# Optimization experiments

Hardware: AMD Instinct MI355X
Metric: run time of the kernel (lower is better)

## Reference

```python
import jax, jax.numpy as jnp
import numpy as np

B, N, D_OBS, D_MSG, H = 4096, 64, 128, 64, 4
HD = D_MSG // H
EPS = 1e-5


def setup_inputs() -> dict:
    key = jax.random.key(0)
    ks = jax.random.split(key, 16)
    def w(k, shape):
        fan_in = shape[0]
        return (jax.random.normal(k, shape, dtype=jnp.float32) / np.sqrt(fan_in)).astype(jnp.float32)
    return {
        'obs_all': jax.random.normal(ks[0], (B, N, D_OBS), dtype=jnp.float32),
        # msg encoder: Linear(obs,128) -> ReLU -> Linear(128,msg)
        'enc_w1': w(ks[1], (D_OBS, 128)), 'enc_b1': jnp.zeros((128,), jnp.float32),
        'enc_w2': w(ks[2], (128, D_MSG)), 'enc_b2': jnp.zeros((D_MSG,), jnp.float32),
        # MultiheadAttention in/out projections (stored as (in, out))
        'in_proj_w': w(ks[3], (D_MSG, 3 * D_MSG)), 'in_proj_b': jnp.zeros((3 * D_MSG,), jnp.float32),
        'out_w': w(ks[4], (D_MSG, D_MSG)), 'out_b': jnp.zeros((D_MSG,), jnp.float32),
        # integrator: Linear(obs+msg,256) -> LayerNorm(256) -> ReLU -> Linear(256,obs)
        'int_w1': w(ks[5], (D_OBS + D_MSG, 256)), 'int_b1': jnp.zeros((256,), jnp.float32),
        'ln_g': jnp.ones((256,), jnp.float32), 'ln_b': jnp.zeros((256,), jnp.float32),
        'int_w2': w(ks[6], (256, D_OBS)), 'int_b2': jnp.zeros((D_OBS,), jnp.float32),
    }


def reference(obs_all, enc_w1, enc_b1, enc_w2, enc_b2,
              in_proj_w, in_proj_b, out_w, out_b,
              int_w1, int_b1, ln_g, ln_b, int_w2, int_b2):
    # --- send: encode observations into messages (B, N, msg_dim) ---
    h = jax.nn.relu(obs_all @ enc_w1 + enc_b1)
    msgs = h @ enc_w2 + enc_b2

    # --- attention aggregation: per-agent query over all messages.
    # The original per-agent loop (query = msgs[:, i:i+1]) is exactly
    # batched self-attention over the agent axis.
    qkv = msgs @ in_proj_w + in_proj_b            # (B, N, 3*msg)
    q, k, v = jnp.split(qkv, 3, axis=-1)
    q = q.reshape(B, N, H, HD)
    k = k.reshape(B, N, H, HD)
    v = v.reshape(B, N, H, HD)
    scale = 1.0 / np.sqrt(HD)
    scores = jnp.einsum('bqhd,bkhd->bhqk', q, k) * scale   # (B, H, N, N)
    attn = jax.nn.softmax(scores, axis=-1)
    ctx = jnp.einsum('bhqk,bkhd->bqhd', attn, v).reshape(B, N, D_MSG)
    agg = ctx @ out_w + out_b                     # (B, N, msg_dim)

    # --- receive: concat obs + aggregated message, MLP with LayerNorm ---
    combined = jnp.concatenate([obs_all, agg], axis=-1)
    z = combined @ int_w1 + int_b1                # (B, N, 256)
    mu = jnp.mean(z, axis=-1, keepdims=True)
    var = jnp.var(z, axis=-1, keepdims=True)
    z = (z - mu) * jax.lax.rsqrt(var + EPS) * ln_g + ln_b
    enriched = jax.nn.relu(z) @ int_w2 + int_b2   # (B, N, obs_dim)
    return enriched, msgs
```

## Files before the change

kernel.cpp:

```cpp
#include <hip/hip_runtime.h>


typedef __attribute__((ext_vector_type(8))) short bf16x8;
typedef __attribute__((ext_vector_type(4))) float f32x4;
typedef __attribute__((ext_vector_type(16))) float f32x16;

#define MFMA16(a, b, c) __builtin_amdgcn_mfma_f32_16x16x32_bf16((a), (b), (c), 0, 0, 0)
#define MFMA32(a, b, c) __builtin_amdgcn_mfma_f32_32x32x16_bf16((a), (b), (c), 0, 0, 0)

__device__ __forceinline__ float b2f(short s) {
    union { unsigned u; float f; } x;
    x.u = ((unsigned)(unsigned short)s) << 16;
    return x.f;
}
__device__ __forceinline__ short f2b(float f) {
    union { float f; unsigned u; } x;
    x.f = f;
    unsigned r = (x.u + 0x7FFFu + ((x.u >> 16) & 1u)) >> 16;
    return (short)r;
}
__device__ __forceinline__ float ldw(const void* p, long i, bool bf) {
    return bf ? b2f(((const short*)p)[i]) : ((const float*)p)[i];
}
__device__ __forceinline__ bf16x8 ld8rt(const void* p, long i, bool bf) {
    if (bf) return *(const bf16x8*)((const short*)p + i);
    const float4* f = (const float4*)((const float*)p + i);
    float4 a = f[0], c = f[1];
    bf16x8 r;
    r[0] = f2b(a.x); r[1] = f2b(a.y); r[2] = f2b(a.z); r[3] = f2b(a.w);
    r[4] = f2b(c.x); r[5] = f2b(c.y); r[6] = f2b(c.z); r[7] = f2b(c.w);
    return r;
}

#define P_S   0
#define H_S   0
#define Z_S   0
#define Q2_S  9216
#define K2_S  13312
#define VT_S  17408
#define LN_S  17408
#define MU_S  18432
#define CTX_S 22016
#define SMEM_SHORTS 26624
#define HP 136
#define MP 72
#define ZP 264
#define PP 72
#define VP 72

#define WT1_OFF   0
#define WT2_OFF   16384
#define WT26_OFF  24576
#define WTI1_OFF  49152
#define WTF_OFF   81920
#define WTI2_OFF  98304
#define WT_TOTAL  131072
#define FB_B26 0
#define FB_BI  192
#define FB_EB1 448
#define FB_EB2 576
#define FB_LG  640
#define FB_LB  896
#define FB_IB2 1152
#define FB_TOTAL 1280
#define OBS_ELEMS 33554432L
#define WS_NEEDED ((unsigned long)(128 + WT_TOTAL + 2 * FB_TOTAL + OBS_ELEMS) * 2UL)

template<bool DO_CONV>
__global__ void prep(const void* __restrict__ obs,
                     const void* __restrict__ w1, const void* __restrict__ w2,
                     const void* __restrict__ wq, const void* __restrict__ wo,
                     const void* __restrict__ wi1, const void* __restrict__ wi2,
                     const void* __restrict__ eb1, const void* __restrict__ eb2,
                     const void* __restrict__ ipb, const void* __restrict__ ob,
                     const void* __restrict__ ib1, const void* __restrict__ lg,
                     const void* __restrict__ lb,  const void* __restrict__ ib2,
                     int* __restrict__ flag, short* __restrict__ wt,
                     float* __restrict__ fb, short* __restrict__ obs_bf) {
    const unsigned short* o16 = (const unsigned short*)obs;
    int lane = threadIdx.x & 63;
    int cnt = 0;
    for (int i = lane; i < 512; i += 64) {
        unsigned e = (o16[i] >> 7) & 0xFFu;
        cnt += (e == 0u || (e >= 80u && e <= 140u)) ? 1 : 0;
    }
#pragma unroll
    for (int off = 1; off < 64; off <<= 1) cnt += __shfl_xor(cnt, off);
    const bool bf = (cnt >= 480);
    if (blockIdx.x == 0 && threadIdx.x == 0) *flag = bf ? 1 : 0;

    long id = (long)blockIdx.x * 256 + threadIdx.x;
    if (id < 16384) {
        int n = (int)id >> 7, k = (int)id & 127;
        wt[WT1_OFF + id] = f2b(ldw(w1, k * 128 + n, bf));
    } else if (id < 24576) {
        int loc = (int)id - 16384, n = loc >> 7, k = loc & 127;
        wt[WT2_OFF + loc] = f2b(ldw(w2, k * 64 + n, bf));
    } else if (id < 49152) {
        int loc = (int)id - 24576, n = loc >> 7, k = loc & 127;
        float s = 0.f;
        for (int j = 0; j < 64; ++j) s += ldw(w2, k * 64 + j, bf) * ldw(wq, j * 192 + n, bf);
        wt[WT26_OFF + loc] = f2b(s);
    } else if (id < 81920) {
        int loc = (int)id - 49152, n = loc >> 7, k = loc & 127;
        wt[WTI1_OFF + loc] = f2b(ldw(wi1, k * 256 + n, bf));
    } else if (id < 98304) {
        int loc = (int)id - 81920, n = loc >> 6, c = loc & 63;
        float s = 0.f;
        for (int m = 0; m < 64; ++m) s += ldw(wo, c * 64 + m, bf) * ldw(wi1, (128 + m) * 256 + n, bf);
        wt[WTF_OFF + loc] = f2b(s);
    } else if (id < 131072) {
        int loc = (int)id - 98304, n = loc >> 8, k = loc & 255;
        wt[WTI2_OFF + loc] = f2b(ldw(wi2, k * 128 + n, bf));
    } else if (id < 131264) {
        int n = (int)id - 131072;
        float s = ldw(ipb, n, bf);
        for (int j = 0; j < 64; ++j) s += ldw(eb2, j, bf) * ldw(wq, j * 192 + n, bf);
        fb[FB_B26 + n] = s;
    } else if (id < 131520) {
        int n = (int)id - 131264;
        float s = ldw(ib1, n, bf);
        for (int m = 0; m < 64; ++m) s += ldw(ob, m, bf) * ldw(wi1, (128 + m) * 256 + n, bf);
        fb[FB_BI + n] = s;
    } else if (id < 132352) {
        int j = (int)id - 131520;
        float v; int d;
        if (j < 128)      { v = ldw(eb1, j, bf);       d = FB_EB1 + j; }
        else if (j < 192) { v = ldw(eb2, j - 128, bf); d = FB_EB2 + j - 128; }
        else if (j < 448) { v = ldw(lg, j - 192, bf);  d = FB_LG + j - 192; }
        else if (j < 704) { v = ldw(lb, j - 448, bf);  d = FB_LB + j - 448; }
        else              { v = ldw(ib2, j - 704, bf); d = FB_IB2 + j - 704; }
        fb[d] = v;
    } else if (DO_CONV && !bf) {
        long base = (id - 132352) * 8;
        if (base < OBS_ELEMS) {
            const float4* f = (const float4*)((const float*)obs + base);
            float4 a = f[0], c = f[1];
            bf16x8 r;
            r[0] = f2b(a.x); r[1] = f2b(a.y); r[2] = f2b(a.z); r[3] = f2b(a.w);
            r[4] = f2b(c.x); r[5] = f2b(c.y); r[6] = f2b(c.z); r[7] = f2b(c.w);
            *(bf16x8*)(obs_bf + base) = r;
        }
    }
}

template<bool OBSBF>
__global__ __launch_bounds__(256, 3)
void macs_main(const void* __restrict__ obs, const int* __restrict__ flag,
               const short* __restrict__ wt, const float* __restrict__ fb,
               const short* __restrict__ obs_bf, void* __restrict__ out) {
    __shared__ __align__(16) short smem[SMEM_SHORTS];
    const int tid = threadIdx.x;
    const int w = tid >> 6;
    const int lane = tid & 63;
    const int q = lane >> 4;
    const int t = lane & 15;
    const int l31 = lane & 31;
    const int hi = lane >> 5;
    const int b = blockIdx.x;
    const long obase = (long)b * 64 * 128;
    const bool inbf = (*flag != 0);
    const bool f32out = !inbf;
    const short* osrc = OBSBF ? (inbf ? (const short*)obs : obs_bf) : (const short*)0;

    bf16x8 oa[4][4];
#pragma unroll
    for (int ks = 0; ks < 4; ++ks)
#pragma unroll
        for (int mt = 0; mt < 4; ++mt) {
            long idx = obase + (mt * 16 + t) * 128 + ks * 32 + q * 8;
            oa[ks][mt] = OBSBF ? *(const bf16x8*)(osrc + idx) : ld8rt(obs, idx, inbf);
        }

    bf16x8 w2p[4];
    bf16x8 wi1p[2][4];
    bf16x8 w2pp[8][2];

    {
        f32x4 acc[4][2] = {};
        const short* wt1p = wt + WT1_OFF;
#pragma unroll
        for (int ks = 0; ks < 4; ++ks) {
            bf16x8 bb[2];
#pragma unroll
            for (int tj = 0; tj < 2; ++tj)
                bb[tj] = *(const bf16x8*)(wt1p + (w * 32 + tj * 16 + t) * 128 + ks * 32 + q * 8);
#pragma unroll
            for (int mt = 0; mt < 4; ++mt)
#pragma unroll
                for (int tj = 0; tj < 2; ++tj)
                    acc[mt][tj] = MFMA16(oa[ks][mt], bb[tj], acc[mt][tj]);
        }
        {
            const short* wt2 = wt + WT2_OFF;
#pragma unroll
            for (int ks = 0; ks < 4; ++ks)
                w2p[ks] = *(const bf16x8*)(wt2 + (w * 16 + t) * 128 + ks * 32 + q * 8);
            __builtin_amdgcn_sched_barrier(0);
        }
        short* hs = smem + H_S;
#pragma unroll
        for (int tj = 0; tj < 2; ++tj) {
            int c = w * 32 + tj * 16 + t;
            float bias = fb[FB_EB1 + c];
#pragma unroll
            for (int mt = 0; mt < 4; ++mt)
#pragma unroll
                for (int i = 0; i < 4; ++i)
                    hs[(mt * 16 + q * 4 + i) * HP + c] = f2b(fmaxf(acc[mt][tj][i] + bias, 0.f));
        }
    }
    __syncthreads();

    {
        const short* hs = smem + H_S;
        const long msgs_base = 33554432L;
        f32x4 am[4] = {};
#pragma unroll
        for (int ks = 0; ks < 4; ++ks) {
            bf16x8 a[4];
#pragma unroll
            for (int mt = 0; mt < 4; ++mt)
                a[mt] = *(const bf16x8*)(hs + (mt * 16 + t) * HP + ks * 32 + q * 8);
#pragma unroll
            for (int mt = 0; mt < 4; ++mt)
                am[mt] = MFMA16(a[mt], w2p[ks], am[mt]);
        }
        float mb = fb[FB_EB2 + w * 16 + t];
        if (f32out) {
#pragma unroll
            for (int mt = 0; mt < 4; ++mt)
#pragma unroll
                for (int i = 0; i < 4; ++i)
                    ((float*)out)[msgs_base + ((long)b * 64 + mt * 16 + q * 4 + i) * 64 + w * 16 + t] = am[mt][i] + mb;
        } else {
#pragma unroll
            for (int mt = 0; mt < 4; ++mt)
#pragma unroll
                for (int i = 0; i < 4; ++i)
                    ((short*)out)[msgs_base + ((long)b * 64 + mt * 16 + q * 4 + i) * 64 + w * 16 + t] = f2b(am[mt][i] + mb);
        }
        f32x4 aq[4][3] = {};
        const short* w26 = wt + WT26_OFF;
#pragma unroll
        for (int ks = 0; ks < 4; ++ks) {
            bf16x8 a[4], bb[3];
#pragma unroll
            for (int mt = 0; mt < 4; ++mt)
                a[mt] = *(const bf16x8*)(hs + (mt * 16 + t) * HP + ks * 32 + q * 8);
#pragma unroll
            for (int tj = 0; tj < 3; ++tj)
                bb[tj] = *(const bf16x8*)(w26 + (w * 48 + tj * 16 + t) * 128 + ks * 32 + q * 8);
#pragma unroll
            for (int mt = 0; mt < 4; ++mt)
#pragma unroll
                for (int tj = 0; tj < 3; ++tj)
                    aq[mt][tj] = MFMA16(a[mt], bb[tj], aq[mt][tj]);
        }
#pragma unroll
        for (int tj = 0; tj < 3; ++tj) {
            int c = w * 48 + tj * 16 + t;
            float bias = fb[FB_B26 + c];
            int sec = c >> 6;
            int head = (c >> 4) & 3;
            float scale = (sec == 0) ? 0.25f : 1.0f;
#pragma unroll
            for (int mt = 0; mt < 4; ++mt)
#pragma unroll
                for (int i = 0; i < 4; ++i) {
                    int r = mt * 16 + q * 4 + i;
                    short bv = f2b((aq[mt][tj][i] + bias) * scale);
                    int idx;
                    if (sec == 0)      idx = Q2_S + head * 1024 + r * 16 + t;
                    else if (sec == 1) idx = K2_S + head * 1024 + r * 16 + t;
                    else               idx = VT_S + head * 1152 + t * VP + r;
                    smem[idx] = bv;
                }
        }
    }
    __syncthreads();

    {
        const int rh = w & 1;
        short* Pq = smem + P_S + w * 2304;
        short* cs = smem + CTX_S;
        bf16x8 ones = { (short)0x3F80, (short)0x3F80, (short)0x3F80, (short)0x3F80,
                        (short)0x3F80, (short)0x3F80, (short)0x3F80, (short)0x3F80 };
#pragma unroll
        for (int p = 0; p < 2; ++p) {
            const int hd = p * 2 + (w >> 1);
            const short* qh = smem + Q2_S + hd * 1024;
            const short* kh = smem + K2_S + hd * 1024;
            const short* vh = smem + VT_S + hd * 1152;
            f32x16 sc0 = {}, sc1 = {};
            {
                bf16x8 aq  = *(const bf16x8*)(qh + (rh * 32 + l31) * 16 + hi * 8);
                bf16x8 bk0 = *(const bf16x8*)(kh + l31 * 16 + hi * 8);
                bf16x8 bk1 = *(const bf16x8*)(kh + (32 + l31) * 16 + hi * 8);
                sc0 = MFMA32(aq, bk0, sc0);
                sc1 = MFMA32(aq, bk1, sc1);
            }
#pragma unroll
            for (int i = 0; i < 16; ++i) {
                int lr = (i & 3) + 8 * (i >> 2) + 4 * hi;
                Pq[lr * PP + l31]      = f2b(__expf(sc0[i]));
                Pq[lr * PP + 32 + l31] = f2b(__expf(sc1[i]));
            }
            f32x4 cx[2] = {}, sm[2] = {};
#pragma unroll
            for (int ks = 0; ks < 2; ++ks) {
                bf16x8 bb = *(const bf16x8*)(vh + t * VP + ks * 32 + q * 8);
                bf16x8 a0 = *(const bf16x8*)(Pq + t * PP + ks * 32 + q * 8);
                bf16x8 a1 = *(const bf16x8*)(Pq + (16 + t) * PP + ks * 32 + q * 8);
                cx[0] = MFMA16(a0, bb, cx[0]);
                cx[1] = MFMA16(a1, bb, cx[1]);
                sm[0] = MFMA16(a0, ones, sm[0]);
                sm[1] = MFMA16(a1, ones, sm[1]);
            }
#pragma unroll
            for (int mt = 0; mt < 2; ++mt)
#pragma unroll
                for (int i = 0; i < 4; ++i) {
                    float inv = __builtin_amdgcn_rcpf(sm[mt][i]);
                    cs[(rh * 32 + mt * 16 + q * 4 + i) * MP + hd * 16 + t] = f2b(cx[mt][i] * inv);
                }
        }
        {
            const short* wti1 = wt + WTI1_OFF;
#pragma unroll
            for (int ks = 0; ks < 2; ++ks)
#pragma unroll
                for (int tj = 0; tj < 4; ++tj)
                    wi1p[ks][tj] = *(const bf16x8*)(wti1 + (w * 64 + tj * 16 + t) * 128 + ks * 32 + q * 8);
            __builtin_amdgcn_sched_barrier(0);
        }
    }
    __syncthreads();

    {
        f32x4 acc[4][4] = {};
        const short* wti1 = wt + WTI1_OFF;
        const short* wtf  = wt + WTF_OFF;
        const short* cs = smem + CTX_S;
#pragma unroll
        for (int ks = 0; ks < 4; ++ks) {
            bf16x8 bb[4];
            if (ks < 2) {
#pragma unroll
                for (int tj = 0; tj < 4; ++tj) bb[tj] = wi1p[ks][tj];
            } else {
#pragma unroll
                for (int tj = 0; tj < 4; ++tj)
                    bb[tj] = *(const bf16x8*)(wti1 + (w * 64 + tj * 16 + t) * 128 + ks * 32 + q * 8);
            }
#pragma unroll
            for (int mt = 0; mt < 4; ++mt)
#pragma unroll
                for (int tj = 0; tj < 4; ++tj)
                    acc[mt][tj] = MFMA16(oa[ks][mt], bb[tj], acc[mt][tj]);
        }
#pragma unroll
        for (int ks = 0; ks < 2; ++ks) {
            bf16x8 a[4], bb[4];
#pragma unroll
            for (int mt = 0; mt < 4; ++mt)
                a[mt] = *(const bf16x8*)(cs + (mt * 16 + t) * MP + ks * 32 + q * 8);
#pragma unroll
            for (int tj = 0; tj < 4; ++tj)
                bb[tj] = *(const bf16x8*)(wtf + (w * 64 + tj * 16 + t) * 64 + ks * 32 + q * 8);
#pragma unroll
            for (int mt = 0; mt < 4; ++mt)
#pragma unroll
                for (int tj = 0; tj < 4; ++tj)
                    acc[mt][tj] = MFMA16(a[mt], bb[tj], acc[mt][tj]);
        }
#pragma unroll
        for (int tj = 0; tj < 4; ++tj) {
            float bias = fb[FB_BI + w * 64 + tj * 16 + t];
#pragma unroll
            for (int mt = 0; mt < 4; ++mt)
#pragma unroll
                for (int i = 0; i < 4; ++i) acc[mt][tj][i] += bias;
        }
        float2* lnred = (float2*)(smem + LN_S);
#pragma unroll
        for (int mt = 0; mt < 4; ++mt)
#pragma unroll
            for (int i = 0; i < 4; ++i) {
                float s = 0.f, s2 = 0.f;
#pragma unroll
                for (int tj = 0; tj < 4; ++tj) {
                    float v = acc[mt][tj][i];
                    s += v;
                    s2 += v * v;
                }
#pragma unroll
                for (int off = 1; off < 16; off <<= 1) {
                    s += __shfl_xor(s, off);
                    s2 += __shfl_xor(s2, off);
                }
                if (t == 0) {
                    float2 p; p.x = s; p.y = s2;
                    lnred[(mt * 16 + q * 4 + i) * 4 + w] = p;
                }
            }
        __syncthreads();
        float2* munr = (float2*)(smem + MU_S);
        if (tid < 64) {
            float S = 0.f, S2 = 0.f;
#pragma unroll
            for (int j = 0; j < 4; ++j) {
                float2 p = lnred[tid * 4 + j];
                S += p.x;
                S2 += p.y;
            }
            float mu = S * (1.f / 256.f);
            float var = S2 * (1.f / 256.f) - mu * mu;
            float2 m; m.x = mu; m.y = rsqrtf(fmaxf(var, 0.f) + 1e-5f);
            munr[tid] = m;
        }
        __syncthreads();
        {
            const short* wti2 = wt + WTI2_OFF;
#pragma unroll
            for (int ks = 0; ks < 8; ++ks)
#pragma unroll
                for (int tj = 0; tj < 2; ++tj)
                    w2pp[ks][tj] = *(const bf16x8*)(wti2 + (w * 32 + tj * 16 + t) * 256 + ks * 32 + q * 8);
            __builtin_amdgcn_sched_barrier(0);
        }
        short* zs = smem + Z_S;
        float gv[4], bv[4];
#pragma unroll
        for (int tj = 0; tj < 4; ++tj) {
            gv[tj] = fb[FB_LG + w * 64 + tj * 16 + t];
            bv[tj] = fb[FB_LB + w * 64 + tj * 16 + t];
        }
#pragma unroll
        for (int mt = 0; mt < 4; ++mt)
#pragma unroll
            for (int i = 0; i < 4; ++i) {
                int r = mt * 16 + q * 4 + i;
                float2 mr = munr[r];
#pragma unroll
                for (int tj = 0; tj < 4; ++tj) {
                    float v = (acc[mt][tj][i] - mr.x) * mr.y * gv[tj] + bv[tj];
                    zs[r * ZP + w * 64 + tj * 16 + t] = f2b(fmaxf(v, 0.f));
                }
            }
    }
    __syncthreads();

    {
        f32x4 acc[4][2] = {};
        const short* zs = smem + Z_S;
#pragma unroll
        for (int ks = 0; ks < 8; ++ks) {
            bf16x8 a[4];
#pragma unroll
            for (int mt = 0; mt < 4; ++mt)
                a[mt] = *(const bf16x8*)(zs + (mt * 16 + t) * ZP + ks * 32 + q * 8);
#pragma unroll
            for (int mt = 0; mt < 4; ++mt)
#pragma unroll
                for (int tj = 0; tj < 2; ++tj)
                    acc[mt][tj] = MFMA16(a[mt], w2pp[ks][tj], acc[mt][tj]);
        }
        if (f32out) {
#pragma unroll
            for (int tj = 0; tj < 2; ++tj) {
                int c = w * 32 + tj * 16 + t;
                float bias = fb[FB_IB2 + c];
#pragma unroll
                for (int mt = 0; mt < 4; ++mt)
#pragma unroll
                    for (int i = 0; i < 4; ++i)
                        ((float*)out)[((long)b * 64 + mt * 16 + q * 4 + i) * 128 + c] = acc[mt][tj][i] + bias;
            }
        } else {
#pragma unroll
            for (int tj = 0; tj < 2; ++tj) {
                int c = w * 32 + tj * 16 + t;
                float bias = fb[FB_IB2 + c];
#pragma unroll
                for (int mt = 0; mt < 4; ++mt)
#pragma unroll
                    for (int i = 0; i < 4; ++i)
                        ((short*)out)[((long)b * 64 + mt * 16 + q * 4 + i) * 128 + c] = f2b(acc[mt][tj][i] + bias);
            }
        }
    }
}

extern "C" void kernel_launch(void* const* d_in, const int* in_sizes, int n_in,
                              void* d_out, int out_size, void* d_ws, size_t ws_size,
                              hipStream_t stream) {
    const void* obs = d_in[0];
    const void* w1  = d_in[1];
    const void* b1  = d_in[2];
    const void* w2  = d_in[3];
    const void* b2  = d_in[4];
    const void* wq  = d_in[5];
    const void* bq  = d_in[6];
    const void* wo  = d_in[7];
    const void* bo  = d_in[8];
    const void* wi1 = d_in[9];
    const void* bi1 = d_in[10];
    const void* lg  = d_in[11];
    const void* lb  = d_in[12];
    const void* wi2 = d_in[13];
    const void* bi2 = d_in[14];
    int* flag = (int*)d_ws;
    short* wt = (short*)d_ws + 128;
    float* fb = (float*)((short*)d_ws + 128 + WT_TOTAL);
    short* obs_bf = (short*)d_ws + 128 + WT_TOTAL + 2 * FB_TOTAL;
    const bool big = (ws_size >= WS_NEEDED);

    if (big) {
        prep<true><<<dim3(16901), dim3(256), 0, stream>>>(
            obs, w1, w2, wq, wo, wi1, wi2, b1, b2, bq, bo, bi1, lg, lb, bi2,
            flag, wt, fb, obs_bf);
        macs_main<true><<<dim3(4096), dim3(256), 0, stream>>>(obs, flag, wt, fb, obs_bf, d_out);
    } else {
        prep<false><<<dim3(517), dim3(256), 0, stream>>>(
            obs, w1, w2, wq, wo, wi1, wi2, b1, b2, bq, bo, bi1, lg, lb, bi2,
            flag, wt, fb, obs_bf);
        macs_main<false><<<dim3(4096), dim3(256), 0, stream>>>(obs, flag, wt, fb, obs_bf, d_out);
    }
}
```

Measured before the change: 586.9 us.

## Drop obs bf16 pre-conversion and register-resident weight prefetch; reload obs per GEMM

```diff
diff --git a/kernel.cpp b/kernel.cpp
--- a/kernel.cpp
+++ b/kernel.cpp
@@ -63,10 +63,7 @@
 #define FB_LB  896
 #define FB_IB2 1152
 #define FB_TOTAL 1280
-#define OBS_ELEMS 33554432L
-#define WS_NEEDED ((unsigned long)(128 + WT_TOTAL + 2 * FB_TOTAL + OBS_ELEMS) * 2UL)
-
-template<bool DO_CONV>
+
 __global__ void prep(const void* __restrict__ obs,
                      const void* __restrict__ w1, const void* __restrict__ w2,
                      const void* __restrict__ wq, const void* __restrict__ wo,
@@ -76,7 +73,7 @@
                      const void* __restrict__ ib1, const void* __restrict__ lg,
                      const void* __restrict__ lb,  const void* __restrict__ ib2,
                      int* __restrict__ flag, short* __restrict__ wt,
-                     float* __restrict__ fb, short* __restrict__ obs_bf) {
+                     float* __restrict__ fb) {
     const unsigned short* o16 = (const unsigned short*)obs;
     int lane = threadIdx.x & 63;
     int cnt = 0;
@@ -131,24 +128,13 @@
         else if (j < 704) { v = ldw(lb, j - 448, bf);  d = FB_LB + j - 448; }
         else              { v = ldw(ib2, j - 704, bf); d = FB_IB2 + j - 704; }
         fb[d] = v;
-    } else if (DO_CONV && !bf) {
-        long base = (id - 132352) * 8;
-        if (base < OBS_ELEMS) {
-            const float4* f = (const float4*)((const float*)obs + base);
-            float4 a = f[0], c = f[1];
-            bf16x8 r;
-            r[0] = f2b(a.x); r[1] = f2b(a.y); r[2] = f2b(a.z); r[3] = f2b(a.w);
-            r[4] = f2b(c.x); r[5] = f2b(c.y); r[6] = f2b(c.z); r[7] = f2b(c.w);
-            *(bf16x8*)(obs_bf + base) = r;
-        }
-    }
-}
-
-template<bool OBSBF>
+    }
+}
+
 __global__ __launch_bounds__(256, 3)
 void macs_main(const void* __restrict__ obs, const int* __restrict__ flag,
                const short* __restrict__ wt, const float* __restrict__ fb,
-               const short* __restrict__ obs_bf, void* __restrict__ out) {
+               void* __restrict__ out) {
     __shared__ __align__(16) short smem[SMEM_SHORTS];
     const int tid = threadIdx.x;
     const int w = tid >> 6;
@@ -161,27 +147,16 @@
     const long obase = (long)b * 64 * 128;
     const bool inbf = (*flag != 0);
     const bool f32out = !inbf;
-    const short* osrc = OBSBF ? (inbf ? (const short*)obs : obs_bf) : (const short*)0;
-
-    bf16x8 oa[4][4];
-#pragma unroll
-    for (int ks = 0; ks < 4; ++ks)
-#pragma unroll
-        for (int mt = 0; mt < 4; ++mt) {
-            long idx = obase + (mt * 16 + t) * 128 + ks * 32 + q * 8;
-            oa[ks][mt] = OBSBF ? *(const bf16x8*)(osrc + idx) : ld8rt(obs, idx, inbf);
-        }
-
-    bf16x8 w2p[4];
-    bf16x8 wi1p[2][4];
-    bf16x8 w2pp[8][2];
 
     {
         f32x4 acc[4][2] = {};
         const short* wt1p = wt + WT1_OFF;
 #pragma unroll
         for (int ks = 0; ks < 4; ++ks) {
-            bf16x8 bb[2];
+            bf16x8 a[4], bb[2];
+#pragma unroll
+            for (int mt = 0; mt < 4; ++mt)
+                a[mt] = ld8rt(obs, obase + (mt * 16 + t) * 128 + ks * 32 + q * 8, inbf);
 #pragma unroll
             for (int tj = 0; tj < 2; ++tj)
                 bb[tj] = *(const bf16x8*)(wt1p + (w * 32 + tj * 16 + t) * 128 + ks * 32 + q * 8);
@@ -189,14 +164,7 @@
             for (int mt = 0; mt < 4; ++mt)
 #pragma unroll
                 for (int tj = 0; tj < 2; ++tj)
-                    acc[mt][tj] = MFMA16(oa[ks][mt], bb[tj], acc[mt][tj]);
-        }
-        {
-            const short* wt2 = wt + WT2_OFF;
-#pragma unroll
-            for (int ks = 0; ks < 4; ++ks)
-                w2p[ks] = *(const bf16x8*)(wt2 + (w * 16 + t) * 128 + ks * 32 + q * 8);
-            __builtin_amdgcn_sched_barrier(0);
+                    acc[mt][tj] = MFMA16(a[mt], bb[tj], acc[mt][tj]);
         }
         short* hs = smem + H_S;
 #pragma unroll
@@ -214,18 +182,29 @@
 
     {
         const short* hs = smem + H_S;
+        const short* wt2 = wt + WT2_OFF;
+        const short* w26 = wt + WT26_OFF;
+        f32x4 am[4] = {};
+        f32x4 aq[4][3] = {};
+#pragma unroll
+        for (int ks = 0; ks < 4; ++ks) {
+            bf16x8 a[4], bm, bb[3];
+#pragma unroll
+            for (int mt = 0; mt < 4; ++mt)
+                a[mt] = *(const bf16x8*)(hs + (mt * 16 + t) * HP + ks * 32 + q * 8);
+            bm = *(const bf16x8*)(wt2 + (w * 16 + t) * 128 + ks * 32 + q * 8);
+#pragma unroll
+            for (int tj = 0; tj < 3; ++tj)
+                bb[tj] = *(const bf16x8*)(w26 + (w * 48 + tj * 16 + t) * 128 + ks * 32 + q * 8);
+#pragma unroll
+            for (int mt = 0; mt < 4; ++mt) {
+                am[mt] = MFMA16(a[mt], bm, am[mt]);
+#pragma unroll
+                for (int tj = 0; tj < 3; ++tj)
+                    aq[mt][tj] = MFMA16(a[mt], bb[tj], aq[mt][tj]);
+            }
+        }
         const long msgs_base = 33554432L;
-        f32x4 am[4] = {};
-#pragma unroll
-        for (int ks = 0; ks < 4; ++ks) {
-            bf16x8 a[4];
-#pragma unroll
-            for (int mt = 0; mt < 4; ++mt)
-                a[mt] = *(const bf16x8*)(hs + (mt * 16 + t) * HP + ks * 32 + q * 8);
-#pragma unroll
-            for (int mt = 0; mt < 4; ++mt)
-                am[mt] = MFMA16(a[mt], w2p[ks], am[mt]);
-        }
         float mb = fb[FB_EB2 + w * 16 + t];
         if (f32out) {
 #pragma unroll
@@ -239,23 +218,6 @@
 #pragma unroll
                 for (int i = 0; i < 4; ++i)
                     ((short*)out)[msgs_base + ((long)b * 64 + mt * 16 + q * 4 + i) * 64 + w * 16 + t] = f2b(am[mt][i] + mb);
-        }
-        f32x4 aq[4][3] = {};
-        const short* w26 = wt + WT26_OFF;
-#pragma unroll
-        for (int ks = 0; ks < 4; ++ks) {
-            bf16x8 a[4], bb[3];
-#pragma unroll
-            for (int mt = 0; mt < 4; ++mt)
-                a[mt] = *(const bf16x8*)(hs + (mt * 16 + t) * HP + ks * 32 + q * 8);
-#pragma unroll
-            for (int tj = 0; tj < 3; ++tj)
-                bb[tj] = *(const bf16x8*)(w26 + (w * 48 + tj * 16 + t) * 128 + ks * 32 + q * 8);
-#pragma unroll
-            for (int mt = 0; mt < 4; ++mt)
-#pragma unroll
-                for (int tj = 0; tj < 3; ++tj)
-                    aq[mt][tj] = MFMA16(a[mt], bb[tj], aq[mt][tj]);
         }
 #pragma unroll
         for (int tj = 0; tj < 3; ++tj) {
@@ -294,11 +256,11 @@
             const short* vh = smem + VT_S + hd * 1152;
             f32x16 sc0 = {}, sc1 = {};
             {
-                bf16x8 aq  = *(const bf16x8*)(qh + (rh * 32 + l31) * 16 + hi * 8);
+                bf16x8 aqf = *(const bf16x8*)(qh + (rh * 32 + l31) * 16 + hi * 8);
                 bf16x8 bk0 = *(const bf16x8*)(kh + l31 * 16 + hi * 8);
                 bf16x8 bk1 = *(const bf16x8*)(kh + (32 + l31) * 16 + hi * 8);
-                sc0 = MFMA32(aq, bk0, sc0);
-                sc1 = MFMA32(aq, bk1, sc1);
+                sc0 = MFMA32(aqf, bk0, sc0);
+                sc1 = MFMA32(aqf, bk1, sc1);
             }
 #pragma unroll
             for (int i = 0; i < 16; ++i) {
@@ -325,15 +287,6 @@
                     cs[(rh * 32 + mt * 16 + q * 4 + i) * MP + hd * 16 + t] = f2b(cx[mt][i] * inv);
                 }
         }
-        {
-            const short* wti1 = wt + WTI1_OFF;
-#pragma unroll
-            for (int ks = 0; ks < 2; ++ks)
-#pragma unroll
-                for (int tj = 0; tj < 4; ++tj)
-                    wi1p[ks][tj] = *(const bf16x8*)(wti1 + (w * 64 + tj * 16 + t) * 128 + ks * 32 + q * 8);
-            __builtin_amdgcn_sched_barrier(0);
-        }
     }
     __syncthreads();
 
@@ -344,20 +297,18 @@
         const short* cs = smem + CTX_S;
 #pragma unroll
         for (int ks = 0; ks < 4; ++ks) {
-            bf16x8 bb[4];
-            if (ks < 2) {
-#pragma unroll
-                for (int tj = 0; tj < 4; ++tj) bb[tj] = wi1p[ks][tj];
-            } else {
+            bf16x8 a[4], bb[4];
+#pragma unroll
+            for (int mt = 0; mt < 4; ++mt)
+                a[mt] = ld8rt(obs, obase + (mt * 16 + t) * 128 + ks * 32 + q * 8, inbf);
+#pragma unroll
+            for (int tj = 0; tj < 4; ++tj)
+                bb[tj] = *(const bf16x8*)(wti1 + (w * 64 + tj * 16 + t) * 128 + ks * 32 + q * 8);
+#pragma unroll
+            for (int mt = 0; mt < 4; ++mt)
 #pragma unroll
                 for (int tj = 0; tj < 4; ++tj)
-                    bb[tj] = *(const bf16x8*)(wti1 + (w * 64 + tj * 16 + t) * 128 + ks * 32 + q * 8);
-            }
-#pragma unroll
-            for (int mt = 0; mt < 4; ++mt)
-#pragma unroll
-                for (int tj = 0; tj < 4; ++tj)
-                    acc[mt][tj] = MFMA16(oa[ks][mt], bb[tj], acc[mt][tj]);
+                    acc[mt][tj] = MFMA16(a[mt], bb[tj], acc[mt][tj]);
         }
 #pragma unroll
         for (int ks = 0; ks < 2; ++ks) {
@@ -420,15 +371,6 @@
             munr[tid] = m;
         }
         __syncthreads();
-        {
-            const short* wti2 = wt + WTI2_OFF;
-#pragma unroll
-            for (int ks = 0; ks < 8; ++ks)
-#pragma unroll
-                for (int tj = 0; tj < 2; ++tj)
-                    w2pp[ks][tj] = *(const bf16x8*)(wti2 + (w * 32 + tj * 16 + t) * 256 + ks * 32 + q * 8);
-            __builtin_amdgcn_sched_barrier(0);
-        }
         short* zs = smem + Z_S;
         float gv[4], bv[4];
 #pragma unroll
@@ -453,18 +395,22 @@
 
     {
         f32x4 acc[4][2] = {};
+        const short* wti2 = wt + WTI2_OFF;
         const short* zs = smem + Z_S;
 #pragma unroll
         for (int ks = 0; ks < 8; ++ks) {
-            bf16x8 a[4];
+            bf16x8 a[4], bb[2];
 #pragma unroll
             for (int mt = 0; mt < 4; ++mt)
                 a[mt] = *(const bf16x8*)(zs + (mt * 16 + t) * ZP + ks * 32 + q * 8);
 #pragma unroll
+            for (int tj = 0; tj < 2; ++tj)
+                bb[tj] = *(const bf16x8*)(wti2 + (w * 32 + tj * 16 + t) * 256 + ks * 32 + q * 8);
+#pragma unroll
             for (int mt = 0; mt < 4; ++mt)
 #pragma unroll
                 for (int tj = 0; tj < 2; ++tj)
-                    acc[mt][tj] = MFMA16(a[mt], w2pp[ks][tj], acc[mt][tj]);
+                    acc[mt][tj] = MFMA16(a[mt], bb[tj], acc[mt][tj]);
         }
         if (f32out) {
 #pragma unroll
@@ -513,18 +459,9 @@
     int* flag = (int*)d_ws;
     short* wt = (short*)d_ws + 128;
     float* fb = (float*)((short*)d_ws + 128 + WT_TOTAL);
-    short* obs_bf = (short*)d_ws + 128 + WT_TOTAL + 2 * FB_TOTAL;
-    const bool big = (ws_size >= WS_NEEDED);
-
-    if (big) {
-        prep<true><<<dim3(16901), dim3(256), 0, stream>>>(
-            obs, w1, w2, wq, wo, wi1, wi2, b1, b2, bq, bo, bi1, lg, lb, bi2,
-            flag, wt, fb, obs_bf);
-        macs_main<true><<<dim3(4096), dim3(256), 0, stream>>>(obs, flag, wt, fb, obs_bf, d_out);
-    } else {
-        prep<false><<<dim3(517), dim3(256), 0, stream>>>(
-            obs, w1, w2, wq, wo, wi1, wi2, b1, b2, bq, bo, bi1, lg, lb, bi2,
-            flag, wt, fb, obs_bf);
-        macs_main<false><<<dim3(4096), dim3(256), 0, stream>>>(obs, flag, wt, fb, obs_bf, d_out);
-    }
-}
+
+    prep<<<dim3(517), dim3(256), 0, stream>>>(
+        obs, w1, w2, wq, wo, wi1, wi2, b1, b2, bq, bo, bi1, lg, lb, bi2,
+        flag, wt, fb);
+    macs_main<<<dim3(4096), dim3(256), 0, stream>>>(obs, flag, wt, fb, d_out);
+}
```

Result: no change. 595.2 us (+1.4%).
